# Kernel optimization log

Hardware: AMD Instinct MI355X
Metric: run time of the kernel (lower is better)

Reference implementation:

```python
import jax, jax.numpy as jnp
import numpy as np

B, CIN, COUT, H, W = 8, 64, 64, 128, 128


def conv2d(x, w, b):
    # NCHW x OIHW -> NCHW, stride 1, SAME padding (kernel 3, pad 1)
    y = jax.lax.conv_general_dilated(
        x, w, window_strides=(1, 1), padding='SAME',
        dimension_numbers=('NCHW', 'OIHW', 'NCHW'))
    return y + b[None, :, None, None]


def bilinear_sample(img, py, px):
    # img: [B, C, H, W]; py, px: [B, K, H, W] float sample coords (y, x)
    # Zero padding outside the image (torchvision DeformConv2d semantics).
    Bn, C, Hn, Wn = img.shape
    y0 = jnp.floor(py)
    x0 = jnp.floor(px)
    wy = py - y0  # [B, K, H, W]
    wx = px - x0
    flat = img.reshape(Bn, C, Hn * Wn)

    def corner(yi, xi):
        valid = (yi >= 0) & (yi < Hn) & (xi >= 0) & (xi < Wn)
        yc = jnp.clip(yi, 0, Hn - 1).astype(jnp.int32)
        xc = jnp.clip(xi, 0, Wn - 1).astype(jnp.int32)
        idx = (yc * Wn + xc).reshape(Bn, -1)  # [B, K*H*W]
        g = jax.vmap(lambda f, i: f[:, i])(flat, idx)  # [B, C, K*H*W]
        g = g.reshape(Bn, C, *py.shape[1:])  # [B, C, K, H, W]
        return g * valid[:, None].astype(img.dtype)

    g00 = corner(y0, x0)
    g01 = corner(y0, x0 + 1)
    g10 = corner(y0 + 1, x0)
    g11 = corner(y0 + 1, x0 + 1)
    wy_ = wy[:, None]  # [B, 1, K, H, W]
    wx_ = wx[:, None]
    return (1 - wy_) * ((1 - wx_) * g00 + wx_ * g01) + wy_ * ((1 - wx_) * g10 + wx_ * g11)


def setup_inputs() -> dict:
    key = jax.random.key(0)
    ks = jax.random.split(key, 4)
    x = jax.random.normal(ks[0], (B, CIN, H, W), dtype=jnp.float32)
    # offset conv: in_channels -> 18 (= 2 * 3 * 3), kernel 3, pad 1
    offset_w = jax.random.normal(ks[1], (18, CIN, 3, 3), dtype=jnp.float32) * 0.01
    offset_b = jnp.zeros((18,), dtype=jnp.float32)
    deform_w = jax.random.normal(ks[2], (COUT, CIN, 3, 3), dtype=jnp.float32) * (1.0 / np.sqrt(CIN * 9))
    deform_b = jnp.zeros((COUT,), dtype=jnp.float32)
    return {'x': x, 'offset_w': offset_w, 'offset_b': offset_b,
            'deform_w': deform_w, 'deform_b': deform_b}


def reference(x, offset_w, offset_b, deform_w, deform_b):
    Bn, C, Hn, Wn = x.shape
    # 1) offset conv
    off = conv2d(x, offset_w, offset_b)  # [B, 18, H, W]
    off = off.reshape(Bn, 9, 2, Hn, Wn)  # per kernel position k: (dy, dx)
    dy = off[:, :, 0]  # [B, 9, H, W]
    dx = off[:, :, 1]
    # 2) sampling positions: p0 + p_k + offset (kernel 3x3, pad 1 -> p_k in {-1,0,1})
    k = jnp.arange(9)
    ki = (k // 3 - 1).astype(jnp.float32)[None, :, None, None]
    kj = (k % 3 - 1).astype(jnp.float32)[None, :, None, None]
    py = jnp.arange(Hn, dtype=jnp.float32)[None, None, :, None] + ki + dy
    px = jnp.arange(Wn, dtype=jnp.float32)[None, None, None, :] + kj + dx
    sampled = bilinear_sample(x, py, px)  # [B, C, 9, H, W]
    # 3) conv accumulation over (C, k)
    w = deform_w.reshape(deform_w.shape[0], C, 9)  # [O, C, 9]
    out = jnp.einsum('bckhw,ock->bohw', sampled, w) + deform_b[None, :, None, None]
    return jax.nn.relu(out)
```

## Files before the change

### kernel.cpp

```cpp
#include <hip/hip_runtime.h>
#include <hip/hip_bf16.h>

#define H_ 128
#define W_ 128
#define B_ 8
#define CIN_ 64
#define COUT_ 64

typedef __attribute__((ext_vector_type(8))) short bf16x8;
typedef __attribute__((ext_vector_type(4))) float f32x4;
typedef __attribute__((ext_vector_type(4))) unsigned int u32x4;

static __device__ __forceinline__ unsigned short f2bf(float f) {
  union { float f; unsigned int u; } a; a.f = f;
  unsigned int u = a.u;
  return (unsigned short)((u + 0x7fffu + ((u >> 16) & 1u)) >> 16);
}

static __device__ __forceinline__ unsigned int cvt_pk_bf16(float lo, float hi) {
  unsigned int r;
  asm("v_cvt_pk_bf16_f32 %0, %1, %2" : "=v"(r) : "v"(lo), "v"(hi));
  return r;
}

static __device__ __forceinline__ void unpack8(const bf16x8& q, float g[8]) {
  union { bf16x8 v; unsigned int w[4]; } u; u.v = q;
#pragma unroll
  for (int j = 0; j < 4; ++j) {
    g[2 * j]     = __uint_as_float(u.w[j] << 16);
    g[2 * j + 1] = __uint_as_float(u.w[j] & 0xffff0000u);
  }
}

__global__ __launch_bounds__(256) void prep_w(const float* __restrict__ dw,
    const float* __restrict__ ow, unsigned short* __restrict__ dwt,
    unsigned short* __restrict__ owt) {
  int id = blockIdx.x * 256 + threadIdx.x;
  if (id < 36864) {
    int c = id & 63, o = (id >> 6) & 63, k = id >> 12;
    dwt[id] = f2bf(dw[(o * 64 + c) * 9 + k]);
  } else if (id < 36864 + 18432) {
    int j = id - 36864;
    int c = j & 63, om = (j >> 6) & 31, t = j >> 11;
    owt[j] = f2bf(om < 18 ? ow[(om * 64 + c) * 9 + t] : 0.f);
  }
}


__device__ __forceinline__ void corner8(const float* __restrict__ x,
    const unsigned short* __restrict__ ldsx, int b, int iy, int ix,
    int oy, int ox, int c8, float g[8]) {
  int ly = iy - oy, lx = ix - ox;
  if ((unsigned)ly < 15u && (unsigned)lx < 16u) {
    int pt = (ly << 4) | lx;
    bf16x8 q = *(const bf16x8*)&ldsx[(pt << 6) | ((c8 ^ (pt & 7)) << 3)];
    unpack8(q, g);
  } else if ((unsigned)iy < (unsigned)H_ && (unsigned)ix < (unsigned)W_) {
#pragma unroll
    for (int ci = 0; ci < 8; ++ci)
      g[ci] = x[((b * CIN_ + (c8 << 3) + ci) * H_ + iy) * W_ + ix];
  } else {
#pragma unroll
    for (int ci = 0; ci < 8; ++ci) g[ci] = 0.f;
  }
}

__global__ __launch_bounds__(256, 4) void deform_main(const float* __restrict__ x,
    const unsigned short* __restrict__ owt, const float* __restrict__ ob,
    const unsigned short* __restrict__ dwt, const float* __restrict__ db,
    float* __restrict__ out) {
  __shared__ unsigned short ldsx[240 * 64];
  __shared__ float offs_lds[64][18];

  const int tid = threadIdx.x;
  const int blk = blockIdx.x;
  const int b = blk >> 8;
  const int ty = ((blk >> 4) & 15) << 3;
  const int tx = (blk & 15) << 3;
  const int oy = ty - 3, ox = tx - 4;
  const int lane = tid & 63;
  const int wv = tid >> 6;
  const int pl = lane & 15;
  const int kgrp = lane >> 4;
  const int pwl = (wv << 4) | pl;
  const int pyy = ty + (pwl >> 3), pxx = tx + (pwl & 7);

  {
    int pt = tid;
    if (pt < 240) {
      int gy = oy + (pt >> 4), gx = ox + (pt & 15);
      bool ok = ((unsigned)gy < (unsigned)H_) && ((unsigned)gx < (unsigned)W_);
      int base = ((b * CIN_) * H_ + gy) * W_ + gx;
#pragma unroll
      for (int c8 = 0; c8 < 8; ++c8) {
        float v[8];
#pragma unroll
        for (int ci = 0; ci < 8; ++ci)
          v[ci] = ok ? x[base + ((c8 << 3) + ci) * (H_ * W_)] : 0.f;
        u32x4 sv;
#pragma unroll
        for (int j = 0; j < 4; ++j) sv[j] = cvt_pk_bf16(v[2 * j], v[2 * j + 1]);
        *(u32x4*)&ldsx[(pt << 6) | ((c8 ^ (pt & 7)) << 3)] = sv;
      }
    }
  }
  __syncthreads();

  {
    f32x4 aoff0 = (f32x4){0.f, 0.f, 0.f, 0.f};
    f32x4 aoff1 = (f32x4){0.f, 0.f, 0.f, 0.f};
#pragma unroll
    for (int t = 0; t < 9; ++t) {
      const int ly = (pwl >> 3) + (t / 3) - 1 + 3;
      const int lx = (pwl & 7) + (t % 3) - 1 + 4;
      const int pt = (ly << 4) | lx;
#pragma unroll
      for (int hf = 0; hf < 2; ++hf) {
        const int c8 = (hf << 2) | kgrp;
        bf16x8 bfr = *(const bf16x8*)&ldsx[(pt << 6) | ((c8 ^ (pt & 7)) << 3)];
        bf16x8 a0 = *(const bf16x8*)&owt[(((t << 5) | pl) << 6) | (c8 << 3)];
        bf16x8 a1 = *(const bf16x8*)&owt[(((t << 5) | 16 | pl) << 6) | (c8 << 3)];
        aoff0 = __builtin_amdgcn_mfma_f32_16x16x32_bf16(a0, bfr, aoff0, 0, 0, 0);
        aoff1 = __builtin_amdgcn_mfma_f32_16x16x32_bf16(a1, bfr, aoff1, 0, 0, 0);
      }
    }
#pragma unroll
    for (int j = 0; j < 4; ++j) {
      int o = (kgrp << 2) + j;
      offs_lds[pwl][o] = aoff0[j] + ob[o];
      int o1 = 16 + o;
      if (o1 < 18) offs_lds[pwl][o1] = aoff1[j] + ob[o1];
    }
  }
  __syncthreads();

  f32x4 acc[4];
#pragma unroll
  for (int mt = 0; mt < 4; ++mt) acc[mt] = (f32x4){0.f, 0.f, 0.f, 0.f};

#pragma unroll
  for (int k = 0; k < 9; ++k) {
    float dy = offs_lds[pwl][2 * k];
    float dx = offs_lds[pwl][2 * k + 1];
    float py = (float)(pyy + (k / 3) - 1) + dy;
    float px = (float)(pxx + (k % 3) - 1) + dx;
    float fy = floorf(py), fx = floorf(px);
    int iy = (int)fy, ix = (int)fx;
    float wy = py - fy, wx = px - fx;
    float wy1 = 1.f - wy, wx1 = 1.f - wx;
    float w00 = wy1 * wx1, w01 = wy1 * wx, w10 = wy * wx1, w11 = wy * wx;

#pragma unroll
    for (int hf = 0; hf < 2; ++hf) {
      const int c8 = (hf << 2) | kgrp;
      float g00[8], g01[8], g10[8], g11[8];
      corner8(x, ldsx, b, iy,     ix,     oy, ox, c8, g00);
      corner8(x, ldsx, b, iy,     ix + 1, oy, ox, c8, g01);
      corner8(x, ldsx, b, iy + 1, ix,     oy, ox, c8, g10);
      corner8(x, ldsx, b, iy + 1, ix + 1, oy, ox, c8, g11);
      union { bf16x8 v; u32x4 w; } bfrag;
#pragma unroll
      for (int j = 0; j < 4; ++j) {
        float v0 = fmaf(g11[2 * j], w11, fmaf(g10[2 * j], w10,
                   fmaf(g01[2 * j], w01, g00[2 * j] * w00)));
        float v1 = fmaf(g11[2 * j + 1], w11, fmaf(g10[2 * j + 1], w10,
                   fmaf(g01[2 * j + 1], w01, g00[2 * j + 1] * w00)));
        bfrag.w[j] = cvt_pk_bf16(v0, v1);
      }
#pragma unroll
      for (int mt = 0; mt < 4; ++mt) {
        bf16x8 af = *(const bf16x8*)&dwt[(k << 12) + (((mt << 4) | pl) << 6)
                                         + (hf << 5) + (kgrp << 3)];
        acc[mt] = __builtin_amdgcn_mfma_f32_16x16x32_bf16(af, bfrag.v, acc[mt], 0, 0, 0);
      }
    }
  }

#pragma unroll
  for (int mt = 0; mt < 4; ++mt) {
#pragma unroll
    for (int j = 0; j < 4; ++j) {
      int o = (mt << 4) | (kgrp << 2) | j;
      float v = acc[mt][j] + db[o];
      out[((b * COUT_ + o) * H_ + pyy) * W_ + pxx] = v > 0.f ? v : 0.f;
    }
  }
}

extern "C" void kernel_launch(void* const* d_in, const int* in_sizes, int n_in,
                              void* d_out, int out_size, void* d_ws, size_t ws_size,
                              hipStream_t stream) {
  const float* x  = (const float*)d_in[0];
  const float* ow = (const float*)d_in[1];
  const float* ob = (const float*)d_in[2];
  const float* dw = (const float*)d_in[3];
  const float* db = (const float*)d_in[4];
  float* out = (float*)d_out;

  unsigned short* dwt = (unsigned short*)d_ws;
  unsigned short* owt = (unsigned short*)((char*)d_ws + 73728);

  hipLaunchKernelGGL(prep_w, dim3(216), dim3(256), 0, stream, dw, ow, dwt, owt);
  hipLaunchKernelGGL(deform_main, dim3(2048), dim3(256), 0, stream,
                     x, owt, ob, dwt, db, out);
}
```

Baseline: 208.6 us.

## Branch-free LDS bilinear gather, shuffle offsets, and swizzled block order

```diff
diff --git a/kernel.cpp b/kernel.cpp
--- a/kernel.cpp
+++ b/kernel.cpp
@@ -21,15 +21,6 @@
   unsigned int r;
   asm("v_cvt_pk_bf16_f32 %0, %1, %2" : "=v"(r) : "v"(lo), "v"(hi));
   return r;
-}
-
-static __device__ __forceinline__ void unpack8(const bf16x8& q, float g[8]) {
-  union { bf16x8 v; unsigned int w[4]; } u; u.v = q;
-#pragma unroll
-  for (int j = 0; j < 4; ++j) {
-    g[2 * j]     = __uint_as_float(u.w[j] << 16);
-    g[2 * j + 1] = __uint_as_float(u.w[j] & 0xffff0000u);
-  }
 }
 
 __global__ __launch_bounds__(256) void prep_w(const float* __restrict__ dw,
@@ -47,33 +38,14 @@
 }
 
 
-__device__ __forceinline__ void corner8(const float* __restrict__ x,
-    const unsigned short* __restrict__ ldsx, int b, int iy, int ix,
-    int oy, int ox, int c8, float g[8]) {
-  int ly = iy - oy, lx = ix - ox;
-  if ((unsigned)ly < 15u && (unsigned)lx < 16u) {
-    int pt = (ly << 4) | lx;
-    bf16x8 q = *(const bf16x8*)&ldsx[(pt << 6) | ((c8 ^ (pt & 7)) << 3)];
-    unpack8(q, g);
-  } else if ((unsigned)iy < (unsigned)H_ && (unsigned)ix < (unsigned)W_) {
-#pragma unroll
-    for (int ci = 0; ci < 8; ++ci)
-      g[ci] = x[((b * CIN_ + (c8 << 3) + ci) * H_ + iy) * W_ + ix];
-  } else {
-#pragma unroll
-    for (int ci = 0; ci < 8; ++ci) g[ci] = 0.f;
-  }
-}
-
 __global__ __launch_bounds__(256, 4) void deform_main(const float* __restrict__ x,
     const unsigned short* __restrict__ owt, const float* __restrict__ ob,
     const unsigned short* __restrict__ dwt, const float* __restrict__ db,
     float* __restrict__ out) {
   __shared__ unsigned short ldsx[240 * 64];
-  __shared__ float offs_lds[64][18];
 
   const int tid = threadIdx.x;
-  const int blk = blockIdx.x;
+  const int blk = ((blockIdx.x & 7) << 8) | (blockIdx.x >> 3);
   const int b = blk >> 8;
   const int ty = ((blk >> 4) & 15) << 3;
   const int tx = (blk & 15) << 3;
@@ -106,6 +78,7 @@
   }
   __syncthreads();
 
+  float ow0, ow1, ow2, ow3, owA, owB;
   {
     f32x4 aoff0 = (f32x4){0.f, 0.f, 0.f, 0.f};
     f32x4 aoff1 = (f32x4){0.f, 0.f, 0.f, 0.f};
@@ -124,15 +97,23 @@
         aoff1 = __builtin_amdgcn_mfma_f32_16x16x32_bf16(a1, bfr, aoff1, 0, 0, 0);
       }
     }
-#pragma unroll
-    for (int j = 0; j < 4; ++j) {
-      int o = (kgrp << 2) + j;
-      offs_lds[pwl][o] = aoff0[j] + ob[o];
-      int o1 = 16 + o;
-      if (o1 < 18) offs_lds[pwl][o1] = aoff1[j] + ob[o1];
-    }
-  }
-  __syncthreads();
+    ow0 = aoff0[0] + ob[(kgrp << 2) + 0];
+    ow1 = aoff0[1] + ob[(kgrp << 2) + 1];
+    ow2 = aoff0[2] + ob[(kgrp << 2) + 2];
+    ow3 = aoff0[3] + ob[(kgrp << 2) + 3];
+    owA = aoff1[0] + ob[16];
+    owB = aoff1[1] + ob[17];
+  }
+
+  float dyk[9], dxk[9];
+#pragma unroll
+  for (int k = 0; k < 8; ++k) {
+    int src = ((k >> 1) << 4) | pl;
+    dyk[k] = __shfl((k & 1) ? ow2 : ow0, src, 64);
+    dxk[k] = __shfl((k & 1) ? ow3 : ow1, src, 64);
+  }
+  dyk[8] = __shfl(owA, pl, 64);
+  dxk[8] = __shfl(owB, pl, 64);
 
   f32x4 acc[4];
 #pragma unroll
@@ -140,40 +121,92 @@
 
 #pragma unroll
   for (int k = 0; k < 9; ++k) {
-    float dy = offs_lds[pwl][2 * k];
-    float dx = offs_lds[pwl][2 * k + 1];
-    float py = (float)(pyy + (k / 3) - 1) + dy;
-    float px = (float)(pxx + (k % 3) - 1) + dx;
-    float fy = floorf(py), fx = floorf(px);
-    int iy = (int)fy, ix = (int)fx;
-    float wy = py - fy, wx = px - fx;
-    float wy1 = 1.f - wy, wx1 = 1.f - wx;
-    float w00 = wy1 * wx1, w01 = wy1 * wx, w10 = wy * wx1, w11 = wy * wx;
-
+    bf16x8 af[2][4];
+#pragma unroll
+    for (int hf = 0; hf < 2; ++hf)
+#pragma unroll
+      for (int mt = 0; mt < 4; ++mt)
+        af[hf][mt] = *(const bf16x8*)&dwt[(k << 12) + (((mt << 4) | pl) << 6)
+                                          + (hf << 5) + (kgrp << 3)];
+
+    const float py = (float)(pyy + (k / 3) - 1) + dyk[k];
+    const float px = (float)(pxx + (k % 3) - 1) + dxk[k];
+    const float fy = floorf(py), fx = floorf(px);
+    const int iy = (int)fy, ix = (int)fx;
+    const float wy = py - fy, wx = px - fx;
+    const float wy1 = 1.f - wy, wx1 = 1.f - wx;
+    const bool ry0 = (unsigned)iy < (unsigned)H_;
+    const bool ry1 = (unsigned)(iy + 1) < (unsigned)H_;
+    const bool rx0 = (unsigned)ix < (unsigned)W_;
+    const bool rx1 = (unsigned)(ix + 1) < (unsigned)W_;
+    const float w00 = (ry0 & rx0) ? wy1 * wx1 : 0.f;
+    const float w01 = (ry0 & rx1) ? wy1 * wx : 0.f;
+    const float w10 = (ry1 & rx0) ? wy * wx1 : 0.f;
+    const float w11 = (ry1 & rx1) ? wy * wx : 0.f;
+
+    const int ly = iy - oy, lx = ix - ox;
+    const int lyc = min(max(ly, 0), 13);
+    const int lxc = min(max(lx, 0), 14);
+    const bool oob = (ly != lyc) | (lx != lxc);
+    const int pt00 = (lyc << 4) | lxc;
+
+    float s0[8], s1[8];
 #pragma unroll
     for (int hf = 0; hf < 2; ++hf) {
       const int c8 = (hf << 2) | kgrp;
-      float g00[8], g01[8], g10[8], g11[8];
-      corner8(x, ldsx, b, iy,     ix,     oy, ox, c8, g00);
-      corner8(x, ldsx, b, iy,     ix + 1, oy, ox, c8, g01);
-      corner8(x, ldsx, b, iy + 1, ix,     oy, ox, c8, g10);
-      corner8(x, ldsx, b, iy + 1, ix + 1, oy, ox, c8, g11);
-      union { bf16x8 v; u32x4 w; } bfrag;
+      float* s = hf ? s1 : s0;
+      const unsigned short* l00 = &ldsx[(pt00 << 6) | ((c8 ^ (pt00 & 7)) << 3)];
+      const unsigned short* l01 = &ldsx[((pt00 + 1) << 6) | ((c8 ^ ((pt00 + 1) & 7)) << 3)];
+      const unsigned short* l10 = &ldsx[((pt00 + 16) << 6) | ((c8 ^ ((pt00 + 16) & 7)) << 3)];
+      const unsigned short* l11 = &ldsx[((pt00 + 17) << 6) | ((c8 ^ ((pt00 + 17) & 7)) << 3)];
+      u32x4 q00 = *(const u32x4*)l00;
+      u32x4 q01 = *(const u32x4*)l01;
+      u32x4 q10 = *(const u32x4*)l10;
+      u32x4 q11 = *(const u32x4*)l11;
 #pragma unroll
       for (int j = 0; j < 4; ++j) {
-        float v0 = fmaf(g11[2 * j], w11, fmaf(g10[2 * j], w10,
-                   fmaf(g01[2 * j], w01, g00[2 * j] * w00)));
-        float v1 = fmaf(g11[2 * j + 1], w11, fmaf(g10[2 * j + 1], w10,
-                   fmaf(g01[2 * j + 1], w01, g00[2 * j + 1] * w00)));
-        bfrag.w[j] = cvt_pk_bf16(v0, v1);
-      }
-#pragma unroll
-      for (int mt = 0; mt < 4; ++mt) {
-        bf16x8 af = *(const bf16x8*)&dwt[(k << 12) + (((mt << 4) | pl) << 6)
-                                         + (hf << 5) + (kgrp << 3)];
-        acc[mt] = __builtin_amdgcn_mfma_f32_16x16x32_bf16(af, bfrag.v, acc[mt], 0, 0, 0);
-      }
-    }
+        float e = __uint_as_float(q00[j] << 16) * w00;
+        e = fmaf(__uint_as_float(q01[j] << 16), w01, e);
+        e = fmaf(__uint_as_float(q10[j] << 16), w10, e);
+        e = fmaf(__uint_as_float(q11[j] << 16), w11, e);
+        float o = __uint_as_float(q00[j] & 0xffff0000u) * w00;
+        o = fmaf(__uint_as_float(q01[j] & 0xffff0000u), w01, o);
+        o = fmaf(__uint_as_float(q10[j] & 0xffff0000u), w10, o);
+        o = fmaf(__uint_as_float(q11[j] & 0xffff0000u), w11, o);
+        s[2 * j] = e;
+        s[2 * j + 1] = o;
+      }
+    }
+
+    if (__builtin_expect(__ballot(oob) != 0ull, 0)) {
+      if (oob) {
+        int y0 = min(max(iy, 0), H_ - 1), x0 = min(max(ix, 0), W_ - 1);
+        int y1 = min(max(iy + 1, 0), H_ - 1), x1 = min(max(ix + 1, 0), W_ - 1);
+#pragma unroll
+        for (int hf = 0; hf < 2; ++hf) {
+          float* s = hf ? s1 : s0;
+          const float* xp = x + (size_t)(b * CIN_ + (((hf << 2) | kgrp) << 3)) * (H_ * W_);
+          for (int ci = 0; ci < 8; ++ci) {
+            const float* xc = xp + ci * (H_ * W_);
+            s[ci] = xc[y0 * W_ + x0] * w00 + xc[y0 * W_ + x1] * w01 +
+                    xc[y1 * W_ + x0] * w10 + xc[y1 * W_ + x1] * w11;
+          }
+        }
+      }
+    }
+
+    union { bf16x8 v; u32x4 w; } bf0, bf1;
+#pragma unroll
+    for (int j = 0; j < 4; ++j) {
+      bf0.w[j] = cvt_pk_bf16(s0[2 * j], s0[2 * j + 1]);
+      bf1.w[j] = cvt_pk_bf16(s1[2 * j], s1[2 * j + 1]);
+    }
+#pragma unroll
+    for (int mt = 0; mt < 4; ++mt)
+      acc[mt] = __builtin_amdgcn_mfma_f32_16x16x32_bf16(af[0][mt], bf0.v, acc[mt], 0, 0, 0);
+#pragma unroll
+    for (int mt = 0; mt < 4; ++mt)
+      acc[mt] = __builtin_amdgcn_mfma_f32_16x16x32_bf16(af[1][mt], bf1.v, acc[mt], 0, 0, 0);
   }
 
 #pragma unroll
```

Result: faster. 190.6 us (-8.6%).
